# Optimization experiments

Measured on AMD Instinct MI355X. Metric: run time of the kernel, lower is better.

The kernel has to match this reference:

```python
import jax, jax.numpy as jnp
import numpy as np

ROWS, COLS = 4096, 11008          # out_features, in_features
NCB, CBSIZE, CLEN = 2, 256, 8     # num_codebooks, 2**nbits, in_group_size
RANK = 32
BLOCK = ROWS                      # bolck_size = reference_weight.shape[0]
N_CODES = ROWS * COLS // CLEN     # total number of codebook entries gathered


def setup_inputs() -> dict:
    key = jax.random.key(0)
    k1, k2, k3, k4, k5 = jax.random.split(key, 5)
    codebooks = jax.random.normal(k1, (NCB, CBSIZE, CLEN), dtype=jnp.float32)
    codes = jax.random.randint(k2, (NCB, N_CODES // NCB), 0, CBSIZE, dtype=jnp.int32)
    scales = jax.random.uniform(k3, (COLS, 1), dtype=jnp.float32, minval=0.5, maxval=1.5)
    L = jax.random.normal(k4, (ROWS, RANK), dtype=jnp.float32) * 0.02
    R = jax.random.normal(k5, (RANK, COLS), dtype=jnp.float32) * 0.02
    return {"codebooks": codebooks, "codes": codes, "scales": scales, "L": L, "R": R}


def reference(codebooks, codes, scales, L, R):
    # differentiable_dequantize: per-codebook gather (embedding_bag with 1-elem
    # bags == plain gather), then per-block scale, then reshape back to weight.
    gathered = jax.vmap(lambda cb, c: cb[c])(codebooks, codes)  # (NCB, N/NCB, CLEN)
    blocks = gathered.reshape(-1, BLOCK) * scales               # (COLS, ROWS) * (COLS,1)
    dequant = blocks.reshape(ROWS, COLS)
    # low-rank correction
    return dequant + L @ R
```

## Files before the change

kernel.cpp:

```cpp
#include <hip/hip_runtime.h>
#include <hip/hip_bf16.h>

constexpr int kRows  = 4096;
constexpr int kCols  = 11008;
constexpr int kRank  = 32;
constexpr int kHalfF = 22544384;

constexpr int RT    = 32;
constexpr int CT    = 256;
constexpr int PITCH = 260;

typedef __attribute__((ext_vector_type(8))) short short8;
typedef __attribute__((ext_vector_type(4))) float f32x4;

__device__ __forceinline__ unsigned short bf16_rne(float x) {
    union { float f; unsigned u; } v; v.f = x;
    return (unsigned short)((v.u + 0x7FFFu + ((v.u >> 16) & 1u)) >> 16);
}

__global__ __launch_bounds__(256) void qw_fused(
    const float* __restrict__ codebooks,
    const int*   __restrict__ codes,
    const float* __restrict__ scales,
    const float* __restrict__ Lm,
    const float* __restrict__ Rm,
    float* __restrict__ outp)
{
    __shared__ __attribute__((aligned(16))) float cb_lds[2 * 256 * 8];
    __shared__ __attribute__((aligned(16))) float corr[RT * PITCH];

    const int tid = threadIdx.x;
    const int i0 = blockIdx.y * RT;
    const int j0 = blockIdx.x * CT;

    {
        const float4* src = (const float4*)codebooks;
        float4* dst = (float4*)cb_lds;
        #pragma unroll
        for (int t = 0; t < 4; ++t) dst[tid + t * 256] = src[tid + t * 256];
    }

    {
        const int wave = tid >> 6;
        const int lane = tid & 63;
        const int n16  = lane & 15;
        const int q    = lane >> 4;
        const int kb   = q * 8;

        const float* ap = Lm + (i0 + ((wave & 1) << 4) + n16) * kRank + kb;
        float4 a0 = *(const float4*)ap;
        float4 a1 = *(const float4*)(ap + 4);
        short8 af;
        af[0] = (short)bf16_rne(a0.x); af[1] = (short)bf16_rne(a0.y);
        af[2] = (short)bf16_rne(a0.z); af[3] = (short)bf16_rne(a0.w);
        af[4] = (short)bf16_rne(a1.x); af[5] = (short)bf16_rne(a1.y);
        af[6] = (short)bf16_rne(a1.z); af[7] = (short)bf16_rne(a1.w);

        const int row_base = ((wave & 1) << 4) + q * 4;

        #pragma unroll
        for (int nt = 0; nt < 8; ++nt) {
            const int NT  = ((wave >> 1) << 3) + nt;
            const int col = j0 + NT * 16 + n16;
            const float* bp = Rm + kb * kCols + col;
            short8 bfr;
            #pragma unroll
            for (int t = 0; t < 8; ++t)
                bfr[t] = (short)bf16_rne(bp[t * kCols]);
            f32x4 acc = {0.f, 0.f, 0.f, 0.f};
            acc = __builtin_amdgcn_mfma_f32_16x16x32_bf16(af, bfr, acc, 0, 0, 0);
            const int ccol = NT * 16 + n16;
            #pragma unroll
            for (int r = 0; r < 4; ++r)
                corr[(row_base + r) * PITCH + ccol] = acc[r];
        }
    }

    __syncthreads();

    {
        const int lane4 = (tid & 63) << 2;
        const int rbase = tid >> 6;
        #pragma unroll
        for (int p = 0; p < 8; ++p) {
            const int row = rbase + (p << 2);
            const int f = (i0 + row) * kCols + j0 + lane4;
            const int code = codes[f >> 3];
            const int cb   = (f >= kHalfF) ? 1 : 0;
            const float scale = scales[f >> 12];
            const float4 w = *(const float4*)(cb_lds + (cb << 11) + (code << 3) + (lane4 & 4));
            const float4 c = *(const float4*)(corr + row * PITCH + lane4);
            float4 o;
            o.x = w.x * scale + c.x;
            o.y = w.y * scale + c.y;
            o.z = w.z * scale + c.z;
            o.w = w.w * scale + c.w;
            *(float4*)(outp + f) = o;
        }
    }
}

extern "C" void kernel_launch(void* const* d_in, const int* in_sizes, int n_in,
                              void* d_out, int out_size, void* d_ws, size_t ws_size,
                              hipStream_t stream) {
    const float* codebooks = (const float*)d_in[0];
    const int*   codes     = (const int*)d_in[1];
    const float* scales    = (const float*)d_in[2];
    const float* Lm        = (const float*)d_in[3];
    const float* Rm        = (const float*)d_in[4];
    float* outp            = (float*)d_out;

    dim3 grid(kCols / CT, kRows / RT);
    qw_fused<<<grid, dim3(256), 0, stream>>>(codebooks, codes, scales, Lm, Rm, outp);
}
```

Measured before the change: 232.9 us.

## Precompute bf16 L and transposed R in a prep kernel before fused dequant

Adds a small pre-kernel that converts L to bf16 and R to a transposed bf16 layout (column-major over rank) in workspace. The main kernel then loads MFMA fragments with single 16-byte vector loads instead of eight strided scalar fp32 loads plus per-element rounding, repeated by every block. This cuts redundant conversion and strided global traffic for the low-rank correction, at the cost of an extra kernel launch and a workspace write/read.

```diff
diff --git a/kernel.cpp b/kernel.cpp
--- a/kernel.cpp
+++ b/kernel.cpp
@@ -1,5 +1,4 @@
 #include <hip/hip_runtime.h>
-#include <hip/hip_bf16.h>
 
 constexpr int kRows  = 4096;
 constexpr int kCols  = 11008;
@@ -18,12 +17,43 @@
     return (unsigned short)((v.u + 0x7FFFu + ((v.u >> 16) & 1u)) >> 16);
 }
 
+__global__ __launch_bounds__(256) void prep(
+    const float* __restrict__ Lm,
+    const float* __restrict__ Rm,
+    unsigned short* __restrict__ Lb,
+    unsigned short* __restrict__ Rbt)
+{
+    const int tid = threadIdx.x;
+    const int b   = blockIdx.x;
+    if (b < 43) {
+        const int j = b * 256 + tid;
+        #pragma unroll
+        for (int t = 0; t < 4; ++t) {
+            short8 o;
+            #pragma unroll
+            for (int k = 0; k < 8; ++k)
+                o[k] = (short)bf16_rne(Rm[(t * 8 + k) * kCols + j]);
+            *(short8*)(Rbt + j * kRank + t * 8) = o;
+        }
+    } else {
+        const int t0 = ((b - 43) * 256 + tid) * 8;
+        const float4 a0 = *(const float4*)(Lm + t0);
+        const float4 a1 = *(const float4*)(Lm + t0 + 4);
+        short8 o;
+        o[0] = (short)bf16_rne(a0.x); o[1] = (short)bf16_rne(a0.y);
+        o[2] = (short)bf16_rne(a0.z); o[3] = (short)bf16_rne(a0.w);
+        o[4] = (short)bf16_rne(a1.x); o[5] = (short)bf16_rne(a1.y);
+        o[6] = (short)bf16_rne(a1.z); o[7] = (short)bf16_rne(a1.w);
+        *(short8*)(Lb + t0) = o;
+    }
+}
+
 __global__ __launch_bounds__(256) void qw_fused(
     const float* __restrict__ codebooks,
     const int*   __restrict__ codes,
     const float* __restrict__ scales,
-    const float* __restrict__ Lm,
-    const float* __restrict__ Rm,
+    const unsigned short* __restrict__ Lb,
+    const unsigned short* __restrict__ Rbt,
     float* __restrict__ outp)
 {
     __shared__ __attribute__((aligned(16))) float cb_lds[2 * 256 * 8];
@@ -45,31 +75,24 @@
         const int lane = tid & 63;
         const int n16  = lane & 15;
         const int q    = lane >> 4;
-        const int kb   = q * 8;
 
-        const float* ap = Lm + (i0 + ((wave & 1) << 4) + n16) * kRank + kb;
-        float4 a0 = *(const float4*)ap;
-        float4 a1 = *(const float4*)(ap + 4);
-        short8 af;
-        af[0] = (short)bf16_rne(a0.x); af[1] = (short)bf16_rne(a0.y);
-        af[2] = (short)bf16_rne(a0.z); af[3] = (short)bf16_rne(a0.w);
-        af[4] = (short)bf16_rne(a1.x); af[5] = (short)bf16_rne(a1.y);
-        af[6] = (short)bf16_rne(a1.z); af[7] = (short)bf16_rne(a1.w);
+        const short8 af = *(const short8*)(Lb + (i0 + ((wave & 1) << 4) + n16) * kRank + (q << 3));
 
-        const int row_base = ((wave & 1) << 4) + q * 4;
+        const unsigned short* bbase =
+            Rbt + (size_t)(j0 + ((wave >> 1) << 7) + n16) * kRank + (q << 3);
+        short8 bf[8];
+        #pragma unroll
+        for (int nt = 0; nt < 8; ++nt)
+            bf[nt] = *(const short8*)(bbase + nt * 16 * kRank);
+
+        const int row_base = ((wave & 1) << 4) + (q << 2);
+        const int cbase    = ((wave >> 1) << 7) + n16;
 
         #pragma unroll
         for (int nt = 0; nt < 8; ++nt) {
-            const int NT  = ((wave >> 1) << 3) + nt;
-            const int col = j0 + NT * 16 + n16;
-            const float* bp = Rm + kb * kCols + col;
-            short8 bfr;
-            #pragma unroll
-            for (int t = 0; t < 8; ++t)
-                bfr[t] = (short)bf16_rne(bp[t * kCols]);
             f32x4 acc = {0.f, 0.f, 0.f, 0.f};
-            acc = __builtin_amdgcn_mfma_f32_16x16x32_bf16(af, bfr, acc, 0, 0, 0);
-            const int ccol = NT * 16 + n16;
+            acc = __builtin_amdgcn_mfma_f32_16x16x32_bf16(af, bf[nt], acc, 0, 0, 0);
+            const int ccol = cbase + nt * 16;
             #pragma unroll
             for (int r = 0; r < 4; ++r)
                 corr[(row_base + r) * PITCH + ccol] = acc[r];
@@ -110,6 +133,11 @@
     const float* Rm        = (const float*)d_in[4];
     float* outp            = (float*)d_out;
 
+    unsigned short* Lb  = (unsigned short*)d_ws;
+    unsigned short* Rbt = Lb + kRows * kRank;
+
+    prep<<<dim3(43 + 64), dim3(256), 0, stream>>>(Lm, Rm, Lb, Rbt);
+
     dim3 grid(kCols / CT, kRows / RT);
-    qw_fused<<<grid, dim3(256), 0, stream>>>(codebooks, codes, scales, Lm, Rm, outp);
+    qw_fused<<<grid, dim3(256), 0, stream>>>(codebooks, codes, scales, Lb, Rbt, outp);
 }
```

New measurement: 217.1 us. 6.8% less time.
